# Kernel tuning notes

Hardware: AMD Instinct MI355X
Metric: run time of the kernel (lower is better)

## Reference

```python
import jax, jax.numpy as jnp
import numpy as np

N_NODES = 100000
N_EDGES = 1600000
IN_FEATS = 256
OUT_FEATS = 128


def setup_inputs() -> dict:
    key = jax.random.key(0)
    k1, k2, k3, k4, k5, k6 = jax.random.split(key, 6)
    feat = jax.random.normal(k1, (N_NODES, IN_FEATS), dtype=jnp.float32)
    # xavier_uniform-style scale for the weight
    limit = float(np.sqrt(6.0 / (IN_FEATS + OUT_FEATS)))
    weight = jax.random.uniform(k2, (IN_FEATS, OUT_FEATS), dtype=jnp.float32, minval=-limit, maxval=limit)
    # degree-normalizer scalars per node (positive, like 1/sqrt(deg))
    cj = jax.random.uniform(k3, (N_NODES, 1), dtype=jnp.float32, minval=0.05, maxval=1.0)
    ci = jax.random.uniform(k4, (N_NODES, 1), dtype=jnp.float32, minval=0.05, maxval=1.0)
    src = jax.random.randint(k5, (N_EDGES,), 0, N_NODES, dtype=jnp.int32)
    dst = jax.random.randint(k6, (N_EDGES,), 0, N_NODES, dtype=jnp.int32)
    return {"feat": feat, "weight": weight, "cj": cj, "ci": ci, "src": src, "dst": dst}


def reference(feat, weight, cj, ci, src, dst):
    # dense transform: [N, in] @ [in, out] -> [N, out]
    h = feat @ weight
    # pre-scale by source normalizer (dropout rate 0 -> identity)
    h = h * cj
    # copy_src + sum aggregation: gather messages at src, scatter-sum into dst
    msgs = h[src]  # [E, out]
    agg = jax.ops.segment_sum(msgs, dst, num_segments=N_NODES)  # [N, out]
    # post-scale by destination normalizer
    return agg * ci
```

## Files before the change

### kernel.cpp

```cpp
#include <hip/hip_runtime.h>

#define N_NODES 100000
#define N_EDGES 1600000
#define IN_F 256
#define OUT_F 128
#define E4 (N_EDGES / 4)

#define BUCKETS 256
#define NPB 391
#define CH 8192
#define NCHUNK ((N_EDGES + CH - 1) / CH)
#define CAP 8192

#define GEMM_T 4
#define GEMM_BLOCKS 196
#define GB_BLOCKS (GEMM_BLOCKS + BUCKETS)

typedef short bf16x8 __attribute__((ext_vector_type(8)));
typedef float f32x4 __attribute__((ext_vector_type(4)));

__device__ __forceinline__ unsigned int f2bf(float f) {
    unsigned int u = __float_as_uint(f);
    return (u + 0x7FFFu + ((u >> 16) & 1u)) >> 16;
}
__device__ __forceinline__ unsigned int pack2(float a, float b) {
    return f2bf(a) | (f2bf(b) << 16);
}
__device__ __forceinline__ float bf_lo(unsigned int u) { return __uint_as_float(u << 16); }
__device__ __forceinline__ float bf_hi(unsigned int u) { return __uint_as_float(u & 0xFFFF0000u); }

__global__ __launch_bounds__(512) void part_kernel(const float* __restrict__ W,
                                                   unsigned short* __restrict__ Wfrag,
                                                   const int* __restrict__ src,
                                                   const int* __restrict__ dst,
                                                   int* __restrict__ bucket_cursor,
                                                   uint2* __restrict__ slab) {
    __shared__ int hist[256];
    __shared__ int hstart[256];
    __shared__ int gbase[256];
    __shared__ uint2 stage[CH];

    const int bid = blockIdx.x;
    const int t = threadIdx.x;

    if (bid < 64) {
        int idx = bid * 512 + t;
        int j    = idx & 7;
        int lane = (idx >> 3) & 63;
        int fkt  = idx >> 9;
        int f    = fkt >> 3;
        int kt   = fkt & 7;
        int c    = f * 16 + (lane & 15);
        int k    = kt * 32 + (lane >> 4) * 8 + j;
        Wfrag[idx] = (unsigned short)f2bf(W[k * OUT_F + c]);
    }

    const int e0 = bid * CH;
    int nE = N_EDGES - e0;
    if (nE > CH) nE = CH;

    if (t < 256) hist[t] = 0;
    __syncthreads();

    int dv[16], rk[16];
    const int4* d4 = reinterpret_cast<const int4*>(dst);
    #pragma unroll
    for (int i = 0; i < 4; ++i) {
        int li = t + i * 512;
        int g4 = (e0 >> 2) + li;
        if (li * 4 < nE && g4 < E4) {
            int4 d = d4[g4];
            dv[i*4+0] = d.x; dv[i*4+1] = d.y; dv[i*4+2] = d.z; dv[i*4+3] = d.w;
            rk[i*4+0] = atomicAdd(&hist[d.x / NPB], 1);
            rk[i*4+1] = atomicAdd(&hist[d.y / NPB], 1);
            rk[i*4+2] = atomicAdd(&hist[d.z / NPB], 1);
            rk[i*4+3] = atomicAdd(&hist[d.w / NPB], 1);
        } else {
            dv[i*4+0] = -1; dv[i*4+1] = -1; dv[i*4+2] = -1; dv[i*4+3] = -1;
        }
    }
    __syncthreads();

    int v = 0;
    if (t < 256) { v = hist[t]; hstart[t] = v; }
    __syncthreads();
    #pragma unroll
    for (int off = 1; off < 256; off <<= 1) {
        int u = 0;
        if (t < 256 && t >= off) u = hstart[t - off];
        __syncthreads();
        if (t < 256) hstart[t] += u;
        __syncthreads();
    }
    if (t < 256) {
        int ex = hstart[t] - v;
        if (v > 0) gbase[t] = atomicAdd(&bucket_cursor[t], v);
        hstart[t] = ex;
    }
    __syncthreads();

    const int4* s4 = reinterpret_cast<const int4*>(src);
    #pragma unroll
    for (int i = 0; i < 4; ++i) {
        int li = t + i * 512;
        int g4 = (e0 >> 2) + li;
        if (dv[i*4] >= 0) {
            int4 s = s4[g4];
            stage[hstart[dv[i*4+0] / NPB] + rk[i*4+0]] = make_uint2((unsigned)dv[i*4+0], (unsigned)s.x);
            stage[hstart[dv[i*4+1] / NPB] + rk[i*4+1]] = make_uint2((unsigned)dv[i*4+1], (unsigned)s.y);
            stage[hstart[dv[i*4+2] / NPB] + rk[i*4+2]] = make_uint2((unsigned)dv[i*4+2], (unsigned)s.z);
            stage[hstart[dv[i*4+3] / NPB] + rk[i*4+3]] = make_uint2((unsigned)dv[i*4+3], (unsigned)s.w);
        }
    }
    __syncthreads();

    for (int idx = t; idx < nE; idx += 512) {
        uint2 p = stage[idx];
        int b = (int)p.x / NPB;
        slab[(size_t)b * CAP + gbase[b] + (idx - hstart[b])] = p;
    }
}

__global__ __launch_bounds__(512) void gemm_bin_kernel(const float* __restrict__ feat,
                                                       const unsigned short* __restrict__ Wfrag,
                                                       const float* __restrict__ cj,
                                                       unsigned short* __restrict__ h,
                                                       const uint2* __restrict__ slab,
                                                       const int* __restrict__ bucket_cursor,
                                                       int* __restrict__ offsets,
                                                       int* __restrict__ bin_src) {
    __shared__ __align__(16) char pool[65536 + 8 * 16 * 136 * 2];

    const int bid = blockIdx.x;
    const int tid = threadIdx.x;

    if (bid >= GEMM_BLOCKS) {
        int* hist = (int*)pool;
        int* cur  = hist + 392;
        int* sbuf = cur + 392;
        int* gbsz = sbuf + 512;

        const int b = bid - GEMM_BLOCKS;
        const int nlo = b * NPB;
        int nn = N_NODES - nlo;
        if (nn > NPB) nn = NPB;

        int v = (tid < 256) ? bucket_cursor[tid] : 0;
        sbuf[tid] = v;
        __syncthreads();
        #pragma unroll
        for (int off = 1; off < 512; off <<= 1) {
            int u = (tid >= off) ? sbuf[tid - off] : 0;
            __syncthreads();
            sbuf[tid] += u;
            __syncthreads();
        }
        if (tid == b) { gbsz[0] = sbuf[tid] - v; gbsz[1] = v; }
        if (b == 0 && tid == 0) offsets[N_NODES] = N_EDGES;
        __syncthreads();
        const int gb = gbsz[0];
        const int sz = gbsz[1];
        const uint2* sl = slab + (size_t)b * CAP;

        for (int j = tid; j < 392; j += 512) hist[j] = 0;
        __syncthreads();

        for (int i = tid; i < sz; i += 512) atomicAdd(&hist[(int)sl[i].x - nlo], 1);
        __syncthreads();

        int hv = (tid < 391) ? hist[tid] : 0;
        sbuf[tid] = hv;
        __syncthreads();
        #pragma unroll
        for (int off = 1; off < 512; off <<= 1) {
            int u = (tid >= off) ? sbuf[tid - off] : 0;
            __syncthreads();
            sbuf[tid] += u;
            __syncthreads();
        }
        if (tid < nn) {
            int o = gb + sbuf[tid] - hv;
            offsets[nlo + tid] = o;
            cur[tid] = o;
        }
        __syncthreads();

        for (int i = tid; i < sz; i += 512) {
            uint2 p = sl[i];
            int pos = atomicAdd(&cur[(int)p.x - nlo], 1);
            bin_src[pos] = (int)p.y;
        }
        return;
    }

    unsigned short* wl = (unsigned short*)pool;
    const int wave = tid >> 6;
    const int lane = tid & 63;
    const int r  = lane & 15;
    const int kq = lane >> 4;
    unsigned short* wout = (unsigned short*)(pool + 65536) + wave * (16 * 136);

    float4 fv[16];
    {
        int arow = bid * 512 + wave * 16 + r;
        if (arow >= N_NODES) arow = N_NODES - 1;
        const float4* fr4 = reinterpret_cast<const float4*>(feat + (size_t)arow * IN_F);
        #pragma unroll
        for (int kt = 0; kt < 8; ++kt) {
            fv[2 * kt]     = fr4[kt * 8 + kq * 2];
            fv[2 * kt + 1] = fr4[kt * 8 + kq * 2 + 1];
        }
    }

    {
        const uint4* wsrc = reinterpret_cast<const uint4*>(Wfrag);
        uint4* wdst = reinterpret_cast<uint4*>(wl);
        #pragma unroll
        for (int i = 0; i < 8; ++i) wdst[tid + i * 512] = wsrc[tid + i * 512];
    }
    __syncthreads();

    for (int t = 0; t < GEMM_T; ++t) {
        const int rowbase = bid * 512 + t * 128 + wave * 16;

        bf16x8 a[8];
        #pragma unroll
        for (int kt = 0; kt < 8; ++kt) {
            uint4 au;
            au.x = pack2(fv[2 * kt].x,     fv[2 * kt].y);
            au.y = pack2(fv[2 * kt].z,     fv[2 * kt].w);
            au.z = pack2(fv[2 * kt + 1].x, fv[2 * kt + 1].y);
            au.w = pack2(fv[2 * kt + 1].z, fv[2 * kt + 1].w);
            a[kt] = *reinterpret_cast<bf16x8*>(&au);
        }

        if (t < GEMM_T - 1) {
            int arow = bid * 512 + (t + 1) * 128 + wave * 16 + r;
            if (arow >= N_NODES) arow = N_NODES - 1;
            const float4* fr4 = reinterpret_cast<const float4*>(feat + (size_t)arow * IN_F);
            #pragma unroll
            for (int kt = 0; kt < 8; ++kt) {
                fv[2 * kt]     = fr4[kt * 8 + kq * 2];
                fv[2 * kt + 1] = fr4[kt * 8 + kq * 2 + 1];
            }
        }

        f32x4 acc[8];
        #pragma unroll
        for (int f = 0; f < 8; ++f) acc[f] = (f32x4){0.f, 0.f, 0.f, 0.f};

        #pragma unroll
        for (int kt = 0; kt < 8; ++kt) {
            #pragma unroll
            for (int f = 0; f < 8; ++f) {
                bf16x8 b = *reinterpret_cast<const bf16x8*>(&wl[((f * 8 + kt) * 64 + lane) * 8]);
                acc[f] = __builtin_amdgcn_mfma_f32_16x16x32_bf16(a[kt], b, acc[f], 0, 0, 0);
            }
        }

        int orow[4]; float cjv[4];
        #pragma unroll
        for (int i = 0; i < 4; ++i) {
            orow[i] = rowbase + kq * 4 + i;
            cjv[i] = cj[orow[i] < N_NODES ? orow[i] : 0];
        }

        #pragma unroll
        for (int f = 0; f < 8; ++f) {
            #pragma unroll
            for (int i = 0; i < 4; ++i) {
                wout[(kq * 4 + i) * 136 + f * 16 + r] =
                    (unsigned short)f2bf(acc[f][i] * cjv[i]);
            }
        }
        __syncthreads();

        {
            int row = lane >> 2;
            int ch  = lane & 3;
            int grow = rowbase + row;
            if (grow < N_NODES) {
                uint4* hv = reinterpret_cast<uint4*>(h);
                #pragma unroll
                for (int j = 0; j < 4; ++j) {
                    uint4 vv = *reinterpret_cast<const uint4*>(
                        (const char*)wout + row * 272 + (ch + 4 * j) * 16);
                    hv[(size_t)grow * 16 + ch + 4 * j] = vv;
                }
            }
        }
        __syncthreads();
    }
}

__global__ __launch_bounds__(256) void gather_kernel(const uint4* __restrict__ h4,
                                                     const float* __restrict__ ci,
                                                     const int* __restrict__ offsets,
                                                     const int* __restrict__ bin_src,
                                                     float* __restrict__ out) {
    int node = blockIdx.x * 16 + (threadIdx.x >> 4);
    int lane = threadIdx.x & 15;
    if (node >= N_NODES) return;

    int beg = offsets[node];
    int end = offsets[node + 1];

    float acc[8] = {};
    int i = beg;
    for (; i + 4 <= end; i += 4) {
        int s0 = bin_src[i + 0];
        int s1 = bin_src[i + 1];
        int s2 = bin_src[i + 2];
        int s3 = bin_src[i + 3];
        uint4 v0 = h4[(size_t)s0 * 16 + lane];
        uint4 v1 = h4[(size_t)s1 * 16 + lane];
        uint4 v2 = h4[(size_t)s2 * 16 + lane];
        uint4 v3 = h4[(size_t)s3 * 16 + lane];
        acc[0] += (bf_lo(v0.x) + bf_lo(v1.x)) + (bf_lo(v2.x) + bf_lo(v3.x));
        acc[1] += (bf_hi(v0.x) + bf_hi(v1.x)) + (bf_hi(v2.x) + bf_hi(v3.x));
        acc[2] += (bf_lo(v0.y) + bf_lo(v1.y)) + (bf_lo(v2.y) + bf_lo(v3.y));
        acc[3] += (bf_hi(v0.y) + bf_hi(v1.y)) + (bf_hi(v2.y) + bf_hi(v3.y));
        acc[4] += (bf_lo(v0.z) + bf_lo(v1.z)) + (bf_lo(v2.z) + bf_lo(v3.z));
        acc[5] += (bf_hi(v0.z) + bf_hi(v1.z)) + (bf_hi(v2.z) + bf_hi(v3.z));
        acc[6] += (bf_lo(v0.w) + bf_lo(v1.w)) + (bf_lo(v2.w) + bf_lo(v3.w));
        acc[7] += (bf_hi(v0.w) + bf_hi(v1.w)) + (bf_hi(v2.w) + bf_hi(v3.w));
    }
    for (; i < end; ++i) {
        int s = bin_src[i];
        uint4 v = h4[(size_t)s * 16 + lane];
        acc[0] += bf_lo(v.x); acc[1] += bf_hi(v.x);
        acc[2] += bf_lo(v.y); acc[3] += bf_hi(v.y);
        acc[4] += bf_lo(v.z); acc[5] += bf_hi(v.z);
        acc[6] += bf_lo(v.w); acc[7] += bf_hi(v.w);
    }
    float sc = ci[node];
    float4 o0 = make_float4(acc[0] * sc, acc[1] * sc, acc[2] * sc, acc[3] * sc);
    float4 o1 = make_float4(acc[4] * sc, acc[5] * sc, acc[6] * sc, acc[7] * sc);
    float4* o4 = reinterpret_cast<float4*>(out) + (size_t)node * 32 + lane * 2;
    o4[0] = o0;
    o4[1] = o1;
}

extern "C" void kernel_launch(void* const* d_in, const int* in_sizes, int n_in,
                              void* d_out, int out_size, void* d_ws, size_t ws_size,
                              hipStream_t stream) {
    const float* feat = (const float*)d_in[0];
    const float* W    = (const float*)d_in[1];
    const float* cj   = (const float*)d_in[2];
    const float* ci   = (const float*)d_in[3];
    const int*   src  = (const int*)d_in[4];
    const int*   dst  = (const int*)d_in[5];
    float* out = (float*)d_out;

    const size_t H_BYTES   = (size_t)N_NODES * OUT_F * 2;
    const size_t WT_BYTES  = (size_t)IN_F * OUT_F * 2;
    const size_t OFF_BYTES = (((size_t)(N_NODES + 1) * 4) + 15) & ~(size_t)15;
    const size_t BC_BYTES  = (((size_t)BUCKETS * 4) + 15) & ~(size_t)15;
    const size_t SLAB_BYTES = (size_t)BUCKETS * CAP * 8;

    char* ws = (char*)d_ws;
    unsigned short* h     = (unsigned short*)ws;  ws += H_BYTES;
    unsigned short* Wfrag = (unsigned short*)ws;  ws += WT_BYTES;
    int* offsets        = (int*)ws;   ws += OFF_BYTES;
    int* bucket_cursor  = (int*)ws;   ws += BC_BYTES;
    uint2* slab         = (uint2*)ws; ws += SLAB_BYTES;
    int* bin_src        = (int*)ws;

    hipMemsetAsync(bucket_cursor, 0, (size_t)BUCKETS * 4, stream);

    part_kernel<<<NCHUNK, 512, 0, stream>>>(W, Wfrag, src, dst, bucket_cursor, slab);

    gemm_bin_kernel<<<GB_BLOCKS, 512, 0, stream>>>(feat, Wfrag, cj, h, slab,
                                                   bucket_cursor, offsets, bin_src);

    gather_kernel<<<(N_NODES + 15) / 16, 256, 0, stream>>>((const uint4*)h, ci, offsets, bin_src, out);
}
```

Before: 123.6 us.

## Merge partition and GEMM/binning into one cooperative kernel with work-stealing queue

Fuses the edge-partition kernel and the GEMM/bucket-binning kernel into a single cooperative launch of 256 blocks separated by a grid-wide sync. After the sync, blocks pull bucket-binning and 128-row GEMM tiles from an atomic work counter. Slab entries are packed into 32 bits (local destination index in the high bits, source in the low bits), which halves slab traffic. The aim is to remove one kernel launch boundary and to balance bucket and GEMM work dynamically. In exchange the change adds a grid barrier, depends on cooperative launch residency, and loses the software prefetch of the next GEMM tile's features.

```diff
diff --git a/kernel.cpp b/kernel.cpp
--- a/kernel.cpp
+++ b/kernel.cpp
@@ -1,4 +1,7 @@
 #include <hip/hip_runtime.h>
+#include <hip/hip_cooperative_groups.h>
+
+namespace cg = cooperative_groups;
 
 #define N_NODES 100000
 #define N_EDGES 1600000
@@ -8,13 +11,11 @@
 
 #define BUCKETS 256
 #define NPB 391
-#define CH 8192
-#define NCHUNK ((N_EDGES + CH - 1) / CH)
 #define CAP 8192
-
-#define GEMM_T 4
-#define GEMM_BLOCKS 196
-#define GB_BLOCKS (GEMM_BLOCKS + BUCKETS)
+#define CH2 6272
+
+#define GEMM_TILES 782
+#define NITEMS (BUCKETS + GEMM_TILES)
 
 typedef short bf16x8 __attribute__((ext_vector_type(8)));
 typedef float f32x4 __attribute__((ext_vector_type(4)));
@@ -29,188 +30,117 @@
 __device__ __forceinline__ float bf_lo(unsigned int u) { return __uint_as_float(u << 16); }
 __device__ __forceinline__ float bf_hi(unsigned int u) { return __uint_as_float(u & 0xFFFF0000u); }
 
-__global__ __launch_bounds__(512) void part_kernel(const float* __restrict__ W,
+__global__ __launch_bounds__(512) void mega_kernel(const float* __restrict__ feat,
+                                                   const float* __restrict__ W,
                                                    unsigned short* __restrict__ Wfrag,
+                                                   const float* __restrict__ cj,
+                                                   unsigned short* __restrict__ h,
                                                    const int* __restrict__ src,
                                                    const int* __restrict__ dst,
                                                    int* __restrict__ bucket_cursor,
-                                                   uint2* __restrict__ slab) {
-    __shared__ int hist[256];
-    __shared__ int hstart[256];
-    __shared__ int gbase[256];
-    __shared__ uint2 stage[CH];
-
-    const int bid = blockIdx.x;
-    const int t = threadIdx.x;
-
-    if (bid < 64) {
-        int idx = bid * 512 + t;
-        int j    = idx & 7;
-        int lane = (idx >> 3) & 63;
-        int fkt  = idx >> 9;
-        int f    = fkt >> 3;
-        int kt   = fkt & 7;
-        int c    = f * 16 + (lane & 15);
-        int k    = kt * 32 + (lane >> 4) * 8 + j;
-        Wfrag[idx] = (unsigned short)f2bf(W[k * OUT_F + c]);
-    }
-
-    const int e0 = bid * CH;
-    int nE = N_EDGES - e0;
-    if (nE > CH) nE = CH;
-
-    if (t < 256) hist[t] = 0;
-    __syncthreads();
-
-    int dv[16], rk[16];
-    const int4* d4 = reinterpret_cast<const int4*>(dst);
-    #pragma unroll
-    for (int i = 0; i < 4; ++i) {
-        int li = t + i * 512;
-        int g4 = (e0 >> 2) + li;
-        if (li * 4 < nE && g4 < E4) {
-            int4 d = d4[g4];
-            dv[i*4+0] = d.x; dv[i*4+1] = d.y; dv[i*4+2] = d.z; dv[i*4+3] = d.w;
-            rk[i*4+0] = atomicAdd(&hist[d.x / NPB], 1);
-            rk[i*4+1] = atomicAdd(&hist[d.y / NPB], 1);
-            rk[i*4+2] = atomicAdd(&hist[d.z / NPB], 1);
-            rk[i*4+3] = atomicAdd(&hist[d.w / NPB], 1);
-        } else {
-            dv[i*4+0] = -1; dv[i*4+1] = -1; dv[i*4+2] = -1; dv[i*4+3] = -1;
-        }
-    }
-    __syncthreads();
-
-    int v = 0;
-    if (t < 256) { v = hist[t]; hstart[t] = v; }
-    __syncthreads();
-    #pragma unroll
-    for (int off = 1; off < 256; off <<= 1) {
-        int u = 0;
-        if (t < 256 && t >= off) u = hstart[t - off];
-        __syncthreads();
-        if (t < 256) hstart[t] += u;
-        __syncthreads();
-    }
-    if (t < 256) {
-        int ex = hstart[t] - v;
-        if (v > 0) gbase[t] = atomicAdd(&bucket_cursor[t], v);
-        hstart[t] = ex;
-    }
-    __syncthreads();
-
-    const int4* s4 = reinterpret_cast<const int4*>(src);
-    #pragma unroll
-    for (int i = 0; i < 4; ++i) {
-        int li = t + i * 512;
-        int g4 = (e0 >> 2) + li;
-        if (dv[i*4] >= 0) {
-            int4 s = s4[g4];
-            stage[hstart[dv[i*4+0] / NPB] + rk[i*4+0]] = make_uint2((unsigned)dv[i*4+0], (unsigned)s.x);
-            stage[hstart[dv[i*4+1] / NPB] + rk[i*4+1]] = make_uint2((unsigned)dv[i*4+1], (unsigned)s.y);
-            stage[hstart[dv[i*4+2] / NPB] + rk[i*4+2]] = make_uint2((unsigned)dv[i*4+2], (unsigned)s.z);
-            stage[hstart[dv[i*4+3] / NPB] + rk[i*4+3]] = make_uint2((unsigned)dv[i*4+3], (unsigned)s.w);
-        }
-    }
-    __syncthreads();
-
-    for (int idx = t; idx < nE; idx += 512) {
-        uint2 p = stage[idx];
-        int b = (int)p.x / NPB;
-        slab[(size_t)b * CAP + gbase[b] + (idx - hstart[b])] = p;
-    }
-}
-
-__global__ __launch_bounds__(512) void gemm_bin_kernel(const float* __restrict__ feat,
-                                                       const unsigned short* __restrict__ Wfrag,
-                                                       const float* __restrict__ cj,
-                                                       unsigned short* __restrict__ h,
-                                                       const uint2* __restrict__ slab,
-                                                       const int* __restrict__ bucket_cursor,
-                                                       int* __restrict__ offsets,
-                                                       int* __restrict__ bin_src) {
+                                                   int* __restrict__ wsctr,
+                                                   unsigned int* __restrict__ slab,
+                                                   int* __restrict__ offsets,
+                                                   int* __restrict__ bin_src) {
     __shared__ __align__(16) char pool[65536 + 8 * 16 * 136 * 2];
+    __shared__ int item_sh;
 
     const int bid = blockIdx.x;
     const int tid = threadIdx.x;
 
-    if (bid >= GEMM_BLOCKS) {
-        int* hist = (int*)pool;
-        int* cur  = hist + 392;
-        int* sbuf = cur + 392;
-        int* gbsz = sbuf + 512;
-
-        const int b = bid - GEMM_BLOCKS;
-        const int nlo = b * NPB;
-        int nn = N_NODES - nlo;
-        if (nn > NPB) nn = NPB;
-
-        int v = (tid < 256) ? bucket_cursor[tid] : 0;
-        sbuf[tid] = v;
-        __syncthreads();
+    {
+        int* hist   = (int*)pool;
+        int* hstart = hist + 256;
+        int* gbase  = hstart + 256;
+        unsigned int* stage = (unsigned int*)(gbase + 256);
+        unsigned char* bstage = (unsigned char*)(stage + CH2);
+
+        if (tid < 128) {
+            int idx = bid * 128 + tid;
+            int j    = idx & 7;
+            int lane = (idx >> 3) & 63;
+            int fkt  = idx >> 9;
+            int f    = fkt >> 3;
+            int kt   = fkt & 7;
+            int c    = f * 16 + (lane & 15);
+            int k    = kt * 32 + (lane >> 4) * 8 + j;
+            Wfrag[idx] = (unsigned short)f2bf(W[k * OUT_F + c]);
+        }
+
+        const int e0 = bid * CH2;
+        int nE = N_EDGES - e0;
+        if (nE > CH2) nE = CH2;
+        if (nE < 0) nE = 0;
+
+        if (tid < 256) hist[tid] = 0;
+        __syncthreads();
+
+        int bb[16], rr[16];
+        unsigned int pp[16];
+        const int4* d4 = reinterpret_cast<const int4*>(dst);
+        const int4* s4 = reinterpret_cast<const int4*>(src);
         #pragma unroll
-        for (int off = 1; off < 512; off <<= 1) {
-            int u = (tid >= off) ? sbuf[tid - off] : 0;
-            __syncthreads();
-            sbuf[tid] += u;
-            __syncthreads();
-        }
-        if (tid == b) { gbsz[0] = sbuf[tid] - v; gbsz[1] = v; }
-        if (b == 0 && tid == 0) offsets[N_NODES] = N_EDGES;
-        __syncthreads();
-        const int gb = gbsz[0];
-        const int sz = gbsz[1];
-        const uint2* sl = slab + (size_t)b * CAP;
-
-        for (int j = tid; j < 392; j += 512) hist[j] = 0;
-        __syncthreads();
-
-        for (int i = tid; i < sz; i += 512) atomicAdd(&hist[(int)sl[i].x - nlo], 1);
-        __syncthreads();
-
-        int hv = (tid < 391) ? hist[tid] : 0;
-        sbuf[tid] = hv;
+        for (int i = 0; i < 4; ++i) {
+            int li = tid + i * 512;
+            if (li * 4 < nE) {
+                int4 d = d4[(e0 >> 2) + li];
+                int4 s = s4[(e0 >> 2) + li];
+                int b0 = d.x / NPB, b1 = d.y / NPB, b2 = d.z / NPB, b3 = d.w / NPB;
+                bb[i*4+0] = b0; pp[i*4+0] = ((unsigned)(d.x - b0 * NPB) << 17) | (unsigned)s.x;
+                bb[i*4+1] = b1; pp[i*4+1] = ((unsigned)(d.y - b1 * NPB) << 17) | (unsigned)s.y;
+                bb[i*4+2] = b2; pp[i*4+2] = ((unsigned)(d.z - b2 * NPB) << 17) | (unsigned)s.z;
+                bb[i*4+3] = b3; pp[i*4+3] = ((unsigned)(d.w - b3 * NPB) << 17) | (unsigned)s.w;
+                rr[i*4+0] = atomicAdd(&hist[b0], 1);
+                rr[i*4+1] = atomicAdd(&hist[b1], 1);
+                rr[i*4+2] = atomicAdd(&hist[b2], 1);
+                rr[i*4+3] = atomicAdd(&hist[b3], 1);
+            } else {
+                bb[i*4+0] = -1; bb[i*4+1] = -1; bb[i*4+2] = -1; bb[i*4+3] = -1;
+            }
+        }
+        __syncthreads();
+
+        int v = 0;
+        if (tid < 256) { v = hist[tid]; hstart[tid] = v; }
         __syncthreads();
         #pragma unroll
-        for (int off = 1; off < 512; off <<= 1) {
-            int u = (tid >= off) ? sbuf[tid - off] : 0;
-            __syncthreads();
-            sbuf[tid] += u;
-            __syncthreads();
-        }
-        if (tid < nn) {
-            int o = gb + sbuf[tid] - hv;
-            offsets[nlo + tid] = o;
-            cur[tid] = o;
-        }
-        __syncthreads();
-
-        for (int i = tid; i < sz; i += 512) {
-            uint2 p = sl[i];
-            int pos = atomicAdd(&cur[(int)p.x - nlo], 1);
-            bin_src[pos] = (int)p.y;
-        }
-        return;
-    }
+        for (int off = 1; off < 256; off <<= 1) {
+            int u = 0;
+            if (tid < 256 && tid >= off) u = hstart[tid - off];
+            __syncthreads();
+            if (tid < 256) hstart[tid] += u;
+            __syncthreads();
+        }
+        if (tid < 256) {
+            int ex = hstart[tid] - v;
+            if (v > 0) gbase[tid] = atomicAdd(&bucket_cursor[tid], v);
+            hstart[tid] = ex;
+        }
+        __syncthreads();
+
+        #pragma unroll
+        for (int i = 0; i < 16; ++i) {
+            if (bb[i] >= 0) {
+                int pos = hstart[bb[i]] + rr[i];
+                stage[pos] = pp[i];
+                bstage[pos] = (unsigned char)bb[i];
+            }
+        }
+        __syncthreads();
+
+        for (int idx = tid; idx < nE; idx += 512) {
+            int b = bstage[idx];
+            slab[(size_t)b * CAP + gbase[b] + (idx - hstart[b])] = stage[idx];
+        }
+    }
+
+    cg::this_grid().sync();
 
     unsigned short* wl = (unsigned short*)pool;
     const int wave = tid >> 6;
     const int lane = tid & 63;
     const int r  = lane & 15;
     const int kq = lane >> 4;
-    unsigned short* wout = (unsigned short*)(pool + 65536) + wave * (16 * 136);
-
-    float4 fv[16];
-    {
-        int arow = bid * 512 + wave * 16 + r;
-        if (arow >= N_NODES) arow = N_NODES - 1;
-        const float4* fr4 = reinterpret_cast<const float4*>(feat + (size_t)arow * IN_F);
-        #pragma unroll
-        for (int kt = 0; kt < 8; ++kt) {
-            fv[2 * kt]     = fr4[kt * 8 + kq * 2];
-            fv[2 * kt + 1] = fr4[kt * 8 + kq * 2 + 1];
-        }
-    }
 
     {
         const uint4* wsrc = reinterpret_cast<const uint4*>(Wfrag);
@@ -220,72 +150,137 @@
     }
     __syncthreads();
 
-    for (int t = 0; t < GEMM_T; ++t) {
-        const int rowbase = bid * 512 + t * 128 + wave * 16;
-
-        bf16x8 a[8];
-        #pragma unroll
-        for (int kt = 0; kt < 8; ++kt) {
-            uint4 au;
-            au.x = pack2(fv[2 * kt].x,     fv[2 * kt].y);
-            au.y = pack2(fv[2 * kt].z,     fv[2 * kt].w);
-            au.z = pack2(fv[2 * kt + 1].x, fv[2 * kt + 1].y);
-            au.w = pack2(fv[2 * kt + 1].z, fv[2 * kt + 1].w);
-            a[kt] = *reinterpret_cast<bf16x8*>(&au);
-        }
-
-        if (t < GEMM_T - 1) {
-            int arow = bid * 512 + (t + 1) * 128 + wave * 16 + r;
+    for (;;) {
+        if (tid == 0) item_sh = atomicAdd(wsctr, 1);
+        __syncthreads();
+        const int item = item_sh;
+        if (item >= NITEMS) break;
+
+        if (item < BUCKETS) {
+            int* hist = (int*)(pool + 65536);
+            int* cur  = hist + 392;
+            int* sbuf = cur + 392;
+            int* gbsz = sbuf + 512;
+
+            const int b = item;
+            const int nlo = b * NPB;
+            int nn = N_NODES - nlo;
+            if (nn > NPB) nn = NPB;
+
+            int v = (tid < 256) ? bucket_cursor[tid] : 0;
+            sbuf[tid] = v;
+            __syncthreads();
+            #pragma unroll
+            for (int off = 1; off < 512; off <<= 1) {
+                int u = (tid >= off) ? sbuf[tid - off] : 0;
+                __syncthreads();
+                sbuf[tid] += u;
+                __syncthreads();
+            }
+            if (tid == b) { gbsz[0] = sbuf[tid] - v; gbsz[1] = v; }
+            if (b == 0 && tid == 0) offsets[N_NODES] = N_EDGES;
+            __syncthreads();
+            const int gb = gbsz[0];
+            const int sz = gbsz[1];
+            const unsigned int* sl = slab + (size_t)b * CAP;
+
+            for (int j = tid; j < 392; j += 512) hist[j] = 0;
+            __syncthreads();
+
+            for (int i = tid; i < sz; i += 512) atomicAdd(&hist[sl[i] >> 17], 1);
+            __syncthreads();
+
+            int hv = (tid < 391) ? hist[tid] : 0;
+            sbuf[tid] = hv;
+            __syncthreads();
+            #pragma unroll
+            for (int off = 1; off < 512; off <<= 1) {
+                int u = (tid >= off) ? sbuf[tid - off] : 0;
+                __syncthreads();
+                sbuf[tid] += u;
+                __syncthreads();
+            }
+            if (tid < nn) {
+                int o = gb + sbuf[tid] - hv;
+                offsets[nlo + tid] = o;
+                cur[tid] = o;
+            }
+            __syncthreads();
+
+            for (int i = tid; i < sz; i += 512) {
+                unsigned int p = sl[i];
+                int pos = atomicAdd(&cur[p >> 17], 1);
+                bin_src[pos] = (int)(p & 0x1FFFFu);
+            }
+        } else {
+            const int g = item - BUCKETS;
+            const int rowbase = g * 128 + wave * 16;
+            unsigned short* wout = (unsigned short*)(pool + 65536) + wave * (16 * 136);
+
+            int arow = rowbase + r;
             if (arow >= N_NODES) arow = N_NODES - 1;
             const float4* fr4 = reinterpret_cast<const float4*>(feat + (size_t)arow * IN_F);
+
+            float4 fv[16];
             #pragma unroll
             for (int kt = 0; kt < 8; ++kt) {
                 fv[2 * kt]     = fr4[kt * 8 + kq * 2];
                 fv[2 * kt + 1] = fr4[kt * 8 + kq * 2 + 1];
             }
-        }
-
-        f32x4 acc[8];
-        #pragma unroll
-        for (int f = 0; f < 8; ++f) acc[f] = (f32x4){0.f, 0.f, 0.f, 0.f};
-
-        #pragma unroll
-        for (int kt = 0; kt < 8; ++kt) {
+
+            bf16x8 a[8];
+            #pragma unroll
+            for (int kt = 0; kt < 8; ++kt) {
+                uint4 au;
+                au.x = pack2(fv[2 * kt].x,     fv[2 * kt].y);
+                au.y = pack2(fv[2 * kt].z,     fv[2 * kt].w);
+                au.z = pack2(fv[2 * kt + 1].x, fv[2 * kt + 1].y);
+                au.w = pack2(fv[2 * kt + 1].z, fv[2 * kt + 1].w);
+                a[kt] = *reinterpret_cast<bf16x8*>(&au);
+            }
+
+            f32x4 acc[8];
+            #pragma unroll
+            for (int f = 0; f < 8; ++f) acc[f] = (f32x4){0.f, 0.f, 0.f, 0.f};
+
+            #pragma unroll
+            for (int kt = 0; kt < 8; ++kt) {
+                #pragma unroll
+                for (int f = 0; f < 8; ++f) {
+                    bf16x8 b = *reinterpret_cast<const bf16x8*>(&wl[((f * 8 + kt) * 64 + lane) * 8]);
+                    acc[f] = __builtin_amdgcn_mfma_f32_16x16x32_bf16(a[kt], b, acc[f], 0, 0, 0);
+                }
+            }
+
+            int orow[4]; float cjv[4];
+            #pragma unroll
+            for (int i = 0; i < 4; ++i) {
+                orow[i] = rowbase + kq * 4 + i;
+                cjv[i] = cj[orow[i] < N_NODES ? orow[i] : 0];
+            }
+
             #pragma unroll
             for (int f = 0; f < 8; ++f) {
-                bf16x8 b = *reinterpret_cast<const bf16x8*>(&wl[((f * 8 + kt) * 64 + lane) * 8]);
-                acc[f] = __builtin_amdgcn_mfma_f32_16x16x32_bf16(a[kt], b, acc[f], 0, 0, 0);
-            }
-        }
-
-        int orow[4]; float cjv[4];
-        #pragma unroll
-        for (int i = 0; i < 4; ++i) {
-            orow[i] = rowbase + kq * 4 + i;
-            cjv[i] = cj[orow[i] < N_NODES ? orow[i] : 0];
-        }
-
-        #pragma unroll
-        for (int f = 0; f < 8; ++f) {
-            #pragma unroll
-            for (int i = 0; i < 4; ++i) {
-                wout[(kq * 4 + i) * 136 + f * 16 + r] =
-                    (unsigned short)f2bf(acc[f][i] * cjv[i]);
-            }
-        }
-        __syncthreads();
-
-        {
-            int row = lane >> 2;
-            int ch  = lane & 3;
-            int grow = rowbase + row;
-            if (grow < N_NODES) {
-                uint4* hv = reinterpret_cast<uint4*>(h);
                 #pragma unroll
-                for (int j = 0; j < 4; ++j) {
-                    uint4 vv = *reinterpret_cast<const uint4*>(
-                        (const char*)wout + row * 272 + (ch + 4 * j) * 16);
-                    hv[(size_t)grow * 16 + ch + 4 * j] = vv;
+                for (int i = 0; i < 4; ++i) {
+                    wout[(kq * 4 + i) * 136 + f * 16 + r] =
+                        (unsigned short)f2bf(acc[f][i] * cjv[i]);
+                }
+            }
+            __syncthreads();
+
+            {
+                int row = lane >> 2;
+                int ch  = lane & 3;
+                int grow = rowbase + row;
+                if (grow < N_NODES) {
+                    uint4* hv4 = reinterpret_cast<uint4*>(h);
+                    #pragma unroll
+                    for (int j = 0; j < 4; ++j) {
+                        uint4 vv = *reinterpret_cast<const uint4*>(
+                            (const char*)wout + row * 272 + (ch + 4 * j) * 16);
+                        hv4[(size_t)grow * 16 + ch + 4 * j] = vv;
+                    }
                 }
             }
         }
@@ -352,26 +347,27 @@
     const int*   dst  = (const int*)d_in[5];
     float* out = (float*)d_out;
 
-    const size_t H_BYTES   = (size_t)N_NODES * OUT_F * 2;
-    const size_t WT_BYTES  = (size_t)IN_F * OUT_F * 2;
-    const size_t OFF_BYTES = (((size_t)(N_NODES + 1) * 4) + 15) & ~(size_t)15;
-    const size_t BC_BYTES  = (((size_t)BUCKETS * 4) + 15) & ~(size_t)15;
-    const size_t SLAB_BYTES = (size_t)BUCKETS * CAP * 8;
+    const size_t H_BYTES    = (size_t)N_NODES * OUT_F * 2;
+    const size_t WT_BYTES   = (size_t)IN_F * OUT_F * 2;
+    const size_t OFF_BYTES  = (((size_t)(N_NODES + 1) * 4) + 15) & ~(size_t)15;
+    const size_t CTR_BYTES  = (((size_t)(BUCKETS + 4) * 4) + 15) & ~(size_t)15;
+    const size_t SLAB_BYTES = (size_t)BUCKETS * CAP * 4;
 
     char* ws = (char*)d_ws;
     unsigned short* h     = (unsigned short*)ws;  ws += H_BYTES;
     unsigned short* Wfrag = (unsigned short*)ws;  ws += WT_BYTES;
-    int* offsets        = (int*)ws;   ws += OFF_BYTES;
-    int* bucket_cursor  = (int*)ws;   ws += BC_BYTES;
-    uint2* slab         = (uint2*)ws; ws += SLAB_BYTES;
+    int* offsets        = (int*)ws;           ws += OFF_BYTES;
+    int* bucket_cursor  = (int*)ws;           ws += CTR_BYTES;
+    unsigned int* slab  = (unsigned int*)ws;  ws += SLAB_BYTES;
     int* bin_src        = (int*)ws;
-
-    hipMemsetAsync(bucket_cursor, 0, (size_t)BUCKETS * 4, stream);
-
-    part_kernel<<<NCHUNK, 512, 0, stream>>>(W, Wfrag, src, dst, bucket_cursor, slab);
-
-    gemm_bin_kernel<<<GB_BLOCKS, 512, 0, stream>>>(feat, Wfrag, cj, h, slab,
-                                                   bucket_cursor, offsets, bin_src);
+    int* wsctr          = bucket_cursor + BUCKETS;
+
+    hipMemsetAsync(bucket_cursor, 0, (size_t)(BUCKETS + 4) * 4, stream);
+
+    void* args[] = {(void*)&feat, (void*)&W, (void*)&Wfrag, (void*)&cj, (void*)&h,
+                    (void*)&src, (void*)&dst, (void*)&bucket_cursor, (void*)&wsctr,
+                    (void*)&slab, (void*)&offsets, (void*)&bin_src};
+    hipLaunchCooperativeKernel((void*)mega_kernel, dim3(256), dim3(512), args, 0, stream);
 
     gather_kernel<<<(N_NODES + 15) / 16, 256, 0, stream>>>((const uint4*)h, ci, offsets, bin_src, out);
 }
```

After: 173.9 us. +40.7%, slower.
